# Kernel optimization log

Hardware: AMD Instinct MI355X
Metric: run time of the kernel (lower is better)

## Reference

```python
import jax, jax.numpy as jnp
import numpy as np
from functools import partial

B, T, F, H = 32768, 48, 16, 32  # batch, horizon, feature dim, rnn_size


def setup_inputs() -> dict:
    key = jax.random.key(0)
    ks = jax.random.split(key, 9)
    return {
        "decoder_feature": jax.random.normal(ks[0], (B, T, F), dtype=jnp.float32),
        "decoder_init_input": jax.random.normal(ks[1], (B, 1), dtype=jnp.float32),
        "init_state": jax.random.normal(ks[2], (B, H), dtype=jnp.float32),
        # GRUCell (Keras default reset_after=True): kernel [in_dim, 3H], recurrent [H, 3H], two biases
        "kernel": jax.random.normal(ks[3], (1 + F, 3 * H), dtype=jnp.float32) * 0.1,
        "recurrent_kernel": jax.random.normal(ks[4], (H, 3 * H), dtype=jnp.float32) * 0.1,
        "bias_x": jax.random.normal(ks[5], (3 * H,), dtype=jnp.float32) * 0.1,
        "bias_h": jax.random.normal(ks[6], (3 * H,), dtype=jnp.float32) * 0.1,
        "dense_w": jax.random.normal(ks[7], (H, 1), dtype=jnp.float32) * 0.1,
        "dense_b": jax.random.normal(ks[8], (1,), dtype=jnp.float32) * 0.1,
    }


def reference(decoder_feature, decoder_init_input, init_state,
              kernel, recurrent_kernel, bias_x, bias_h, dense_w, dense_b):
    units = init_state.shape[-1]

    def step(carry, feat_t):
        h, prev_out = carry                              # h: [B,H], prev_out: [B,1]
        x = jnp.concatenate([prev_out, feat_t], axis=1)  # [B, 1+F]
        mx = x @ kernel + bias_x                         # [B, 3H]
        mh = h @ recurrent_kernel + bias_h               # [B, 3H] (reset_after=True)
        xz, xr, xh = jnp.split(mx, 3, axis=1)
        hz, hr, hh_in = jnp.split(mh, 3, axis=1)
        z = jax.nn.sigmoid(xz + hz)
        r = jax.nn.sigmoid(xr + hr)
        hh = jnp.tanh(xh + r * hh_in)
        h_new = z * h + (1.0 - z) * hh                   # GRU output == new state
        out = h_new @ dense_w + dense_b                  # Dense(1): [B,1]
        return (h_new, out), out

    feats = jnp.transpose(decoder_feature, (1, 0, 2))    # [T,B,F] time-major for scan
    _, outs = jax.lax.scan(step, (init_state, decoder_init_input), feats)
    return jnp.transpose(outs, (1, 0, 2))                # [B,T,1]
```

## Files before the change

### kernel.cpp

```cpp
#include <hip/hip_runtime.h>


typedef __attribute__((ext_vector_type(8))) short short8;
typedef __attribute__((ext_vector_type(4))) float f32x4;

constexpr int T_STEPS = 48;
constexpr int F_DIM   = 16;
constexpr int H_DIM   = 32;
constexpr int ROW_SH  = 40;
constexpr int WAVE_SH = 16 * ROW_SH;

union S8 { short8 s; unsigned u[4]; };

__device__ __forceinline__ unsigned pk_bf16(float hi, float lo) {
    return __builtin_amdgcn_perm(__float_as_uint(hi) + 0x8000u,
                                 __float_as_uint(lo) + 0x8000u, 0x07060302u);
}
__device__ __forceinline__ short bf16s(float x) {
    return (short)((__float_as_uint(x) + 0x8000u) >> 16);
}
__device__ __forceinline__ float fsig(float x) {
    return __builtin_amdgcn_rcpf(1.0f + __expf(-x));
}
__device__ __forceinline__ float ftanh(float x) {
    return 1.0f - 2.0f * __builtin_amdgcn_rcpf(__expf(2.0f * x) + 1.0f);
}
#define MFMA(a, b, c) __builtin_amdgcn_mfma_f32_16x16x32_bf16(a, b, c, 0, 0, 0)

__global__ __launch_bounds__(256, 2)
void gru_mfma3(const float* __restrict__ feat,
               const float* __restrict__ init_in,
               const float* __restrict__ init_h,
               const float* __restrict__ Wk,
               const float* __restrict__ Rk,
               const float* __restrict__ bx,
               const float* __restrict__ bh,
               const float* __restrict__ dw,
               const float* __restrict__ db,
               float* __restrict__ out)
{
    __shared__ __align__(16) short hsh[4 * WAVE_SH];
    const int lane = threadIdx.x & 63;
    const int wave = threadIdx.x >> 6;
    const int ln   = lane & 15;
    const int quad = lane >> 4;
    const int b0   = (blockIdx.x * 4 + wave) * 16;
    short* hbW = hsh + wave * WAVE_SH;
    short* hwr = hbW + quad * 4 * ROW_SH + ln;
    const short8* hrd = (const short8*)(hbW + ln * ROW_SH + quad * 8);

    S8 Wf[6], Rf[6], Dwf;
#pragma unroll
    for (int tn = 0; tn < 6; ++tn) {
#pragma unroll
        for (int j = 0; j < 8; ++j) {
            const int k = quad * 8 + j;
            const int n = tn * 16 + ln;
            const float wv = (k < 16) ? Wk[(size_t)(k + 1) * 96 + n] : 0.0f;
            Wf[tn].s[j] = bf16s(wv);
            Rf[tn].s[j] = bf16s(Rk[(size_t)k * 96 + n]);
        }
    }
#pragma unroll
    for (int j = 0; j < 8; ++j) Dwf.s[j] = bf16s(dw[quad * 8 + j]);

    float bzv[2], brv[2], bxhv[2], bhhv[2], wpz[2], wpr[2], wph[2];
#pragma unroll
    for (int tn = 0; tn < 2; ++tn) {
        const int n = tn * 16 + ln;
        bzv[tn]  = bx[n] + bh[n];
        brv[tn]  = bx[32 + n] + bh[32 + n];
        bxhv[tn] = bx[64 + n];
        bhhv[tn] = bh[64 + n];
        wpz[tn]  = Wk[n];
        wpr[tn]  = Wk[32 + n];
        wph[tn]  = Wk[64 + n];
    }
    const float dbs = db[0];
    const f32x4 dbc = {dbs, dbs, dbs, dbs};

    f32x4 hc[2];
#pragma unroll
    for (int tn = 0; tn < 2; ++tn)
#pragma unroll
        for (int i = 0; i < 4; ++i)
            hc[tn][i] = init_h[(size_t)(b0 + quad * 4 + i) * H_DIM + tn * 16 + ln];
    S8 ha;
    {
        const float* hp = init_h + (size_t)(b0 + ln) * H_DIM + quad * 8;
        const f32x4 a = *(const f32x4*)hp;
        const f32x4 b = *(const f32x4*)(hp + 4);
        ha.u[0] = pk_bf16(a[1], a[0]); ha.u[1] = pk_bf16(a[3], a[2]);
        ha.u[2] = pk_bf16(b[1], b[0]); ha.u[3] = pk_bf16(b[3], b[2]);
    }
    f32x4 po;
#pragma unroll
    for (int i = 0; i < 4; ++i) po[i] = init_in[b0 + quad * 4 + i];

    float* outB = out + (size_t)(b0 + quad * 4) * T_STEPS;

    const float* fqb = feat + (size_t)(b0 + ln) * (T_STEPS * F_DIM) + (quad & 1) * 8;
    f32x4 pa = *(const f32x4*)(fqb);
    f32x4 pb = *(const f32x4*)(fqb + 4);

    f32x4 oD = MFMA(ha.s, Dwf.s, dbc);

    for (int t = 0; t < T_STEPS; ++t) {
        if (t > 0) {
            if (ln == 0) {
#pragma unroll
                for (int i = 0; i < 4; ++i) outB[i * T_STEPS + (t - 1)] = oD[i];
            }
            po = oD;
        }

        S8 xa;
        xa.u[0] = pk_bf16(pa[1], pa[0]); xa.u[1] = pk_bf16(pa[3], pa[2]);
        xa.u[2] = pk_bf16(pb[1], pb[0]); xa.u[3] = pk_bf16(pb[3], pb[2]);
        const unsigned zm = (quad < 2) ? 0xFFFFFFFFu : 0u;
        xa.u[0] &= zm; xa.u[1] &= zm; xa.u[2] &= zm; xa.u[3] &= zm;

        const int t1 = (t < T_STEPS - 1) ? t + 1 : T_STEPS - 1;
        pa = *(const f32x4*)(fqb + t1 * F_DIM);
        pb = *(const f32x4*)(fqb + t1 * F_DIM + 4);

        f32x4 aZ[2], aR[2], aXH[2], aHH[2];
#pragma unroll
        for (int tn = 0; tn < 2; ++tn)
#pragma unroll
            for (int i = 0; i < 4; ++i) {
                aZ[tn][i]  = fmaf(po[i], wpz[tn], bzv[tn]);
                aR[tn][i]  = fmaf(po[i], wpr[tn], brv[tn]);
                aXH[tn][i] = fmaf(po[i], wph[tn], bxhv[tn]);
                aHH[tn][i] = bhhv[tn];
            }
#pragma unroll
        for (int tn = 0; tn < 2; ++tn) {
            aZ[tn]  = MFMA(xa.s, Wf[tn].s,     aZ[tn]);
            aZ[tn]  = MFMA(ha.s, Rf[tn].s,     aZ[tn]);
            aR[tn]  = MFMA(xa.s, Wf[2 + tn].s, aR[tn]);
            aR[tn]  = MFMA(ha.s, Rf[2 + tn].s, aR[tn]);
            aXH[tn] = MFMA(xa.s, Wf[4 + tn].s, aXH[tn]);
            aHH[tn] = MFMA(ha.s, Rf[4 + tn].s, aHH[tn]);
        }

#pragma unroll
        for (int tn = 0; tn < 2; ++tn)
#pragma unroll
            for (int i = 0; i < 4; ++i) {
                const float zz = fsig(aZ[tn][i]);
                const float rr = fsig(aR[tn][i]);
                const float cc = ftanh(aXH[tn][i] + rr * aHH[tn][i]);
                const float hn = cc + zz * (hc[tn][i] - cc);
                hc[tn][i] = hn;
                hwr[i * ROW_SH + tn * 16] = bf16s(hn);
            }

        ha.s = *hrd;
        oD = MFMA(ha.s, Dwf.s, dbc);
    }

    if (ln == 0) {
#pragma unroll
        for (int i = 0; i < 4; ++i) outB[i * T_STEPS + (T_STEPS - 1)] = oD[i];
    }
}

extern "C" void kernel_launch(void* const* d_in, const int* in_sizes, int n_in,
                              void* d_out, int out_size, void* d_ws, size_t ws_size,
                              hipStream_t stream) {
    const float* feat    = (const float*)d_in[0];
    const float* init_in = (const float*)d_in[1];
    const float* init_h  = (const float*)d_in[2];
    const float* Wk      = (const float*)d_in[3];
    const float* Rk      = (const float*)d_in[4];
    const float* bx      = (const float*)d_in[5];
    const float* bh      = (const float*)d_in[6];
    const float* dw      = (const float*)d_in[7];
    const float* db      = (const float*)d_in[8];
    float* out           = (float*)d_out;

    const int B = in_sizes[2] / H_DIM;
    dim3 grid((unsigned)(B / 64));
    dim3 block(256);
    hipLaunchKernelGGL(gru_mfma3, grid, block, 0, stream,
                       feat, init_in, init_h, Wk, Rk, bx, bh, dw, db, out);
}
```

Before: 216.4 us.

## Transpose GRU MFMA operands, compute dense output via cross-lane reduction, stage outputs in LDS

Swaps the MFMA operand order so the gate accumulators come out transposed: each lane holds hidden units for one batch row. The Dense(1) projection becomes a per-lane FMA plus a swizzle/bpermute reduction instead of an extra MFMA on the serial critical path. Outputs are buffered in LDS and written once at the end as coalesced float4 stores, replacing per-step scattered global stores. The cost is more LDS per block and extra cross-lane ops each step.

```diff
diff --git a/kernel.cpp b/kernel.cpp
--- a/kernel.cpp
+++ b/kernel.cpp
@@ -8,7 +8,9 @@
 constexpr int F_DIM   = 16;
 constexpr int H_DIM   = 32;
 constexpr int ROW_SH  = 40;
-constexpr int WAVE_SH = 16 * ROW_SH;
+constexpr int H_BYTES = 16 * ROW_SH * 2;
+constexpr int O_FLOATS = 16 * T_STEPS;
+constexpr int WAVE_BYTES = H_BYTES + O_FLOATS * 4;
 
 union S8 { short8 s; unsigned u[4]; };
 
@@ -26,9 +28,10 @@
     return 1.0f - 2.0f * __builtin_amdgcn_rcpf(__expf(2.0f * x) + 1.0f);
 }
 #define MFMA(a, b, c) __builtin_amdgcn_mfma_f32_16x16x32_bf16(a, b, c, 0, 0, 0)
+#define SWZ16(v) __int_as_float(__builtin_amdgcn_ds_swizzle(__float_as_int(v), 0x401F))
 
 __global__ __launch_bounds__(256, 2)
-void gru_mfma3(const float* __restrict__ feat,
+void gru_mfma4(const float* __restrict__ feat,
                const float* __restrict__ init_in,
                const float* __restrict__ init_h,
                const float* __restrict__ Wk,
@@ -39,17 +42,21 @@
                const float* __restrict__ db,
                float* __restrict__ out)
 {
-    __shared__ __align__(16) short hsh[4 * WAVE_SH];
+    __shared__ __align__(16) char lds[4 * WAVE_BYTES];
     const int lane = threadIdx.x & 63;
     const int wave = threadIdx.x >> 6;
     const int ln   = lane & 15;
     const int quad = lane >> 4;
     const int b0   = (blockIdx.x * 4 + wave) * 16;
-    short* hbW = hsh + wave * WAVE_SH;
-    short* hwr = hbW + quad * 4 * ROW_SH + ln;
-    const short8* hrd = (const short8*)(hbW + ln * ROW_SH + quad * 8);
-
-    S8 Wf[6], Rf[6], Dwf;
+
+    char*  my   = lds + wave * WAVE_BYTES;
+    short* hsh  = (short*)my;
+    float* obuf = (float*)(my + H_BYTES);
+    unsigned* hw = (unsigned*)(hsh + ln * ROW_SH + quad * 4);
+    const short8* hr = (const short8*)(hsh + ln * ROW_SH + quad * 8);
+    const int bpa = (lane ^ 32) << 2;
+
+    S8 Wf[6], Rf[6];
 #pragma unroll
     for (int tn = 0; tn < 6; ++tn) {
 #pragma unroll
@@ -61,59 +68,46 @@
             Rf[tn].s[j] = bf16s(Rk[(size_t)k * 96 + n]);
         }
     }
-#pragma unroll
-    for (int j = 0; j < 8; ++j) Dwf.s[j] = bf16s(dw[quad * 8 + j]);
-
-    float bzv[2], brv[2], bxhv[2], bhhv[2], wpz[2], wpr[2], wph[2];
-#pragma unroll
-    for (int tn = 0; tn < 2; ++tn) {
-        const int n = tn * 16 + ln;
-        bzv[tn]  = bx[n] + bh[n];
-        brv[tn]  = bx[32 + n] + bh[32 + n];
-        bxhv[tn] = bx[64 + n];
-        bhhv[tn] = bh[64 + n];
-        wpz[tn]  = Wk[n];
-        wpr[tn]  = Wk[32 + n];
-        wph[tn]  = Wk[64 + n];
-    }
+
+    float bz8[8], br8[8], bxh8[8], bhh8[8], wz8[8], wr8[8], wh8[8], dw8[8];
+#pragma unroll
+    for (int tn = 0; tn < 2; ++tn)
+#pragma unroll
+        for (int i = 0; i < 4; ++i) {
+            const int c = tn * 16 + quad * 4 + i;
+            const int idx = tn * 4 + i;
+            bz8[idx]  = bx[c] + bh[c];
+            br8[idx]  = bx[32 + c] + bh[32 + c];
+            bxh8[idx] = bx[64 + c];
+            bhh8[idx] = bh[64 + c];
+            wz8[idx]  = Wk[c];
+            wr8[idx]  = Wk[32 + c];
+            wh8[idx]  = Wk[64 + c];
+            dw8[idx]  = dw[c];
+        }
     const float dbs = db[0];
-    const f32x4 dbc = {dbs, dbs, dbs, dbs};
-
-    f32x4 hc[2];
+
+    float hc[8];
 #pragma unroll
     for (int tn = 0; tn < 2; ++tn)
 #pragma unroll
         for (int i = 0; i < 4; ++i)
-            hc[tn][i] = init_h[(size_t)(b0 + quad * 4 + i) * H_DIM + tn * 16 + ln];
-    S8 ha;
+            hc[tn * 4 + i] = init_h[(size_t)(b0 + ln) * H_DIM + tn * 16 + quad * 4 + i];
+    S8 hB;
     {
         const float* hp = init_h + (size_t)(b0 + ln) * H_DIM + quad * 8;
         const f32x4 a = *(const f32x4*)hp;
         const f32x4 b = *(const f32x4*)(hp + 4);
-        ha.u[0] = pk_bf16(a[1], a[0]); ha.u[1] = pk_bf16(a[3], a[2]);
-        ha.u[2] = pk_bf16(b[1], b[0]); ha.u[3] = pk_bf16(b[3], b[2]);
-    }
-    f32x4 po;
-#pragma unroll
-    for (int i = 0; i < 4; ++i) po[i] = init_in[b0 + quad * 4 + i];
-
-    float* outB = out + (size_t)(b0 + quad * 4) * T_STEPS;
+        hB.u[0] = pk_bf16(a[1], a[0]); hB.u[1] = pk_bf16(a[3], a[2]);
+        hB.u[2] = pk_bf16(b[1], b[0]); hB.u[3] = pk_bf16(b[3], b[2]);
+    }
+    float po = init_in[b0 + ln];
 
     const float* fqb = feat + (size_t)(b0 + ln) * (T_STEPS * F_DIM) + (quad & 1) * 8;
     f32x4 pa = *(const f32x4*)(fqb);
     f32x4 pb = *(const f32x4*)(fqb + 4);
 
-    f32x4 oD = MFMA(ha.s, Dwf.s, dbc);
-
     for (int t = 0; t < T_STEPS; ++t) {
-        if (t > 0) {
-            if (ln == 0) {
-#pragma unroll
-                for (int i = 0; i < 4; ++i) outB[i * T_STEPS + (t - 1)] = oD[i];
-            }
-            po = oD;
-        }
-
         S8 xa;
         xa.u[0] = pk_bf16(pa[1], pa[0]); xa.u[1] = pk_bf16(pa[3], pa[2]);
         xa.u[2] = pk_bf16(pb[1], pb[0]); xa.u[3] = pk_bf16(pb[3], pb[2]);
@@ -129,40 +123,60 @@
         for (int tn = 0; tn < 2; ++tn)
 #pragma unroll
             for (int i = 0; i < 4; ++i) {
-                aZ[tn][i]  = fmaf(po[i], wpz[tn], bzv[tn]);
-                aR[tn][i]  = fmaf(po[i], wpr[tn], brv[tn]);
-                aXH[tn][i] = fmaf(po[i], wph[tn], bxhv[tn]);
-                aHH[tn][i] = bhhv[tn];
+                const int idx = tn * 4 + i;
+                aZ[tn][i]  = fmaf(po, wz8[idx], bz8[idx]);
+                aR[tn][i]  = fmaf(po, wr8[idx], br8[idx]);
+                aXH[tn][i] = fmaf(po, wh8[idx], bxh8[idx]);
+                aHH[tn][i] = bhh8[idx];
             }
 #pragma unroll
         for (int tn = 0; tn < 2; ++tn) {
-            aZ[tn]  = MFMA(xa.s, Wf[tn].s,     aZ[tn]);
-            aZ[tn]  = MFMA(ha.s, Rf[tn].s,     aZ[tn]);
-            aR[tn]  = MFMA(xa.s, Wf[2 + tn].s, aR[tn]);
-            aR[tn]  = MFMA(ha.s, Rf[2 + tn].s, aR[tn]);
-            aXH[tn] = MFMA(xa.s, Wf[4 + tn].s, aXH[tn]);
-            aHH[tn] = MFMA(ha.s, Rf[4 + tn].s, aHH[tn]);
+            aZ[tn]  = MFMA(Wf[tn].s,     xa.s, aZ[tn]);
+            aZ[tn]  = MFMA(Rf[tn].s,     hB.s, aZ[tn]);
+            aR[tn]  = MFMA(Wf[2 + tn].s, xa.s, aR[tn]);
+            aR[tn]  = MFMA(Rf[2 + tn].s, hB.s, aR[tn]);
+            aXH[tn] = MFMA(Wf[4 + tn].s, xa.s, aXH[tn]);
+            aHH[tn] = MFMA(Rf[4 + tn].s, hB.s, aHH[tn]);
         }
 
+        float hn[8];
+        float partial = 0.0f;
 #pragma unroll
         for (int tn = 0; tn < 2; ++tn)
 #pragma unroll
             for (int i = 0; i < 4; ++i) {
+                const int idx = tn * 4 + i;
                 const float zz = fsig(aZ[tn][i]);
                 const float rr = fsig(aR[tn][i]);
                 const float cc = ftanh(aXH[tn][i] + rr * aHH[tn][i]);
-                const float hn = cc + zz * (hc[tn][i] - cc);
-                hc[tn][i] = hn;
-                hwr[i * ROW_SH + tn * 16] = bf16s(hn);
+                const float h2 = cc + zz * (hc[idx] - cc);
+                hc[idx] = h2;
+                hn[idx] = h2;
+                partial = fmaf(h2, dw8[idx], partial);
             }
 
-        ha.s = *hrd;
-        oD = MFMA(ha.s, Dwf.s, dbc);
-    }
-
-    if (ln == 0) {
-#pragma unroll
-        for (int i = 0; i < 4; ++i) outB[i * T_STEPS + (T_STEPS - 1)] = oD[i];
+        float s1 = partial + SWZ16(partial);
+        s1 += __int_as_float(__builtin_amdgcn_ds_bpermute(bpa, __float_as_int(s1)));
+        const float o = s1 + dbs;
+        if (quad == 0) obuf[t * 16 + ln] = o;
+        po = o;
+
+        hw[0] = pk_bf16(hn[1], hn[0]);
+        hw[1] = pk_bf16(hn[3], hn[2]);
+        hw[8] = pk_bf16(hn[5], hn[4]);
+        hw[9] = pk_bf16(hn[7], hn[6]);
+        hB.s = *hr;
+    }
+
+    const int row = lane >> 2;
+    const int tb  = (lane & 3) * 12;
+    float* orow = out + (size_t)(b0 + row) * T_STEPS + tb;
+#pragma unroll
+    for (int k = 0; k < 3; ++k) {
+        f32x4 v;
+#pragma unroll
+        for (int e = 0; e < 4; ++e) v[e] = obuf[(tb + k * 4 + e) * 16 + row];
+        *(f32x4*)(orow + k * 4) = v;
     }
 }
 
@@ -183,6 +197,6 @@
     const int B = in_sizes[2] / H_DIM;
     dim3 grid((unsigned)(B / 64));
     dim3 block(256);
-    hipLaunchKernelGGL(gru_mfma3, grid, block, 0, stream,
+    hipLaunchKernelGGL(gru_mfma4, grid, block, 0, stream,
                        feat, init_in, init_h, Wk, Rk, bx, bh, dw, db, out);
 }
```

Result: faster. 198.6 us (-8.2%).
